# Kernel tuning notes

Measured on AMD Instinct MI355X. Metric: run time of the kernel, lower is better.

## Reference

```python
import jax, jax.numpy as jnp
import numpy as np
from functools import partial

# norse LIFAdEx default parameters
DT = 0.001
TAU_SYN_INV = 1.0 / 5e-3   # 200.0
TAU_MEM_INV = 1.0 / 1e-2   # 100.0
TAU_ADA_INV = 2.0
ADAPT_CURRENT = 4.0
ADAPT_SPIKE = 0.02
DELTA_T = 0.5
V_LEAK = 0.0
V_TH = 1.0
V_RESET = 0.0
ALPHA = 100.0              # superspike surrogate sharpness
TAU_FILTER_INV = 223.1435511314


@jax.custom_vjp
def superspike(x):
    # forward: heaviside; backward: superspike surrogate grad
    return (x > 0).astype(x.dtype)

def _ss_fwd(x):
    return superspike(x), x

def _ss_bwd(x, g):
    return (g / (ALPHA * jnp.abs(x) + 1.0) ** 2,)

superspike.defvjp(_ss_fwd, _ss_bwd)


def lif_adex_recurrent(x, W_in, W_rec):
    """x: (T,B,F) -> spikes (T,B,H). norse lif_adex_step semantics."""
    T, B, _ = x.shape
    H = W_rec.shape[0]
    # precompute feed-forward input current for all steps: (T,B,H)
    i_in = jnp.einsum('tbf,hf->tbh', x, W_in)

    def step(carry, ic):
        z, v, i, a = carry
        dv = DT * TAU_MEM_INV * ((V_LEAK - v)
                                 + DELTA_T * jnp.exp((v - V_TH) / DELTA_T)
                                 + i - a)
        v_dec = v + dv
        i_dec = i - DT * TAU_SYN_INV * i
        a_dec = a + DT * TAU_ADA_INV * (ADAPT_CURRENT * (v - V_LEAK) - a)
        z_new = superspike(v_dec - V_TH)
        v_new = (1.0 - z_new) * v_dec + z_new * V_RESET
        i_new = i_dec + ic + z @ W_rec.T
        a_new = a_dec + z_new * ADAPT_SPIKE
        return (z_new, v_new, i_new, a_new), z_new

    z0 = jnp.zeros((B, H), x.dtype)
    init = (z0, z0, z0, z0)
    _, spikes = jax.lax.scan(step, init, i_in)
    return spikes


def exp_filter(spikes, W_out, b_out):
    """Linear readout + exponential low-pass filter over time."""
    y = jnp.einsum('tbh,oh->tbo', spikes, W_out) + b_out  # (T,B,O)
    k = DT * TAU_FILTER_INV

    def step(o_prev, y_t):
        o = o_prev + k * (y_t - o_prev)
        return o, o

    o0 = y[0]
    _, rest = jax.lax.scan(step, o0, y[1:])
    return jnp.concatenate([o0[None], rest], axis=0)


def setup_inputs() -> dict:
    key = jax.random.key(0)
    kx, k1, k2, k3, k4 = jax.random.split(key, 5)
    T, B, F, H, O = 500, 128, 128, 512, 32
    x = jax.random.normal(kx, (T, B, F), dtype=jnp.float32)
    W_in = jax.random.normal(k1, (H, F), dtype=jnp.float32) * np.sqrt(2.0 / F)
    W_rec = jax.random.normal(k2, (H, H), dtype=jnp.float32) * np.sqrt(2.0 / H)
    W_out = jax.random.normal(k3, (O, H), dtype=jnp.float32) * np.sqrt(1.0 / H)
    b_out = jax.random.normal(k4, (O,), dtype=jnp.float32) * 0.01
    return {'x': x, 'W_in': W_in, 'W_rec': W_rec, 'W_out': W_out, 'b_out': b_out}


def reference(x, W_in, W_rec, W_out, b_out):
    spikes = lif_adex_recurrent(x, W_in, W_rec)
    return exp_filter(spikes, W_out, b_out)
```

## Files before the change

### kernel.cpp

```cpp
#include <hip/hip_runtime.h>
#include <hip/hip_bf16.h>
#include <cstdint>
#include <cstddef>

#define T_STEPS 500
#define BATCH   128
#define FDIM    128
#define HDIM    512
#define ODIM    32
#define M_ROWS  (T_STEPS * BATCH)
#define ZOFF    (512u << 11)

__device__ __forceinline__ float bfbits2f(unsigned short u) {
    union { unsigned int i; float f; } c; c.i = ((unsigned int)u) << 16; return c.f;
}

__global__ void detect_kernel(const unsigned short* __restrict__ xw, int* __restrict__ flag) {
    __shared__ int cnt;
    if (threadIdx.x == 0) cnt = 0;
    __syncthreads();
    unsigned short w = xw[threadIdx.x * 2];
    int e = (w >> 7) & 0xFF;
    if (e >= 170) atomicAdd(&cnt, 1);
    __syncthreads();
    if (threadIdx.x == 0) *flag = (cnt >= 8) ? 1 : 0;
}

__global__ void prep_kernel(const void* __restrict__ Wrec,
                            const void* __restrict__ Wout,
                            const void* __restrict__ bout,
                            const void* __restrict__ Win,
                            const int* __restrict__ flag,
                            float* __restrict__ WrecT,
                            float* __restrict__ WoutT,
                            float* __restrict__ WinT,
                            float* __restrict__ bout32) {
    const int fp32 = *flag;
    int idx = blockIdx.x * blockDim.x + threadIdx.x;
    if (idx < HDIM * HDIM) {
        int h  = idx / HDIM;
        int hp = idx % HDIM;
        float v = fp32 ? ((const float*)Wrec)[idx]
                       : bfbits2f(((const unsigned short*)Wrec)[idx]);
        WrecT[hp * HDIM + h] = v;
    }
    if (idx < HDIM) WrecT[HDIM * HDIM + idx] = 0.f;
    if (idx < ODIM * HDIM) {
        int o = idx / HDIM;
        int h = idx % HDIM;
        float v = fp32 ? ((const float*)Wout)[idx]
                       : bfbits2f(((const unsigned short*)Wout)[idx]);
        WoutT[h * ODIM + o] = v;
    }
    if (idx < HDIM * FDIM) {
        int h = idx / FDIM;
        int f = idx % FDIM;
        float v = fp32 ? ((const float*)Win)[idx]
                       : bfbits2f(((const unsigned short*)Win)[idx]);
        WinT[f * HDIM + h] = v;
    }
    if (idx < ODIM) {
        bout32[idx] = fp32 ? ((const float*)bout)[idx]
                           : bfbits2f(((const unsigned short*)bout)[idx]);
    }
}

__global__ __launch_bounds__(256) void iin_gemm(const void* __restrict__ x,
                                                const float* __restrict__ WinT,
                                                const int* __restrict__ flag,
                                                float* __restrict__ iin) {
    const int fp32 = *flag;
    const int tid  = threadIdx.x;
    const int m0   = blockIdx.x * 32;

    __shared__ float xs[32][FDIM];

    for (int i = tid; i < 32 * FDIM; i += 256) {
        size_t g = (size_t)m0 * FDIM + i;
        xs[0][i] = fp32 ? ((const float*)x)[g]
                        : bfbits2f(((const unsigned short*)x)[g]);
    }
    __syncthreads();

    float acc[32][2];
#pragma unroll
    for (int m = 0; m < 32; ++m) { acc[m][0] = 0.f; acc[m][1] = 0.f; }

#pragma unroll 4
    for (int k = 0; k < FDIM; ++k) {
        float w0 = WinT[(size_t)k * HDIM + tid];
        float w1 = WinT[(size_t)k * HDIM + 256 + tid];
#pragma unroll
        for (int m = 0; m < 32; ++m) {
            float xv = xs[m][k];
            acc[m][0] += xv * w0;
            acc[m][1] += xv * w1;
        }
    }

#pragma unroll
    for (int m = 0; m < 32; ++m) {
        iin[(size_t)(m0 + m) * HDIM + tid]       = acc[m][0];
        iin[(size_t)(m0 + m) * HDIM + 256 + tid] = acc[m][1];
    }
}

__global__ __launch_bounds__(1024) void scan_kernel(const float* __restrict__ iin,
                                                    const float* __restrict__ WrecT,
                                                    unsigned long long* __restrict__ masksG) {
    const int b    = blockIdx.x;
    const int tid  = threadIdx.x;
    const int q    = tid & 127;
    const int p    = tid >> 7;
    const int lane = tid & 63;
    const int wv   = tid >> 6;
    const bool st  = tid < HDIM;
    const int h    = tid;

    __shared__ unsigned long long wmask[8];
    __shared__ float4 part[8][128];
    __shared__ alignas(16) unsigned int slA[8][68];
    __shared__ alignas(16) unsigned int slB[8][68];
    unsigned int (*slO)[68] = slA;
    unsigned int (*slN)[68] = slB;

    const float kDvC  = 0.1f;
    const float kSyn  = 0.2f;
    const float kAda  = 0.002f;

    float v = 0.f, cur = 0.f, a = 0.f;
    int   cnt = 0;
    const char* WQ = (const char*)WrecT + q * 16;

    for (int t = 0; t < T_STEPS; ++t) {
        float ic = 0.f, i_dec = 0.f;
        bool  zk = false;
        unsigned long long m = 0;

        if (st) {
            ic = iin[((size_t)t * BATCH + b) * HDIM + h];
            float s = (0.0f - v) + 0.5f * expf((v - 1.0f) * 2.0f);
            s = s + cur;
            s = s - a;
            float v_dec = v + kDvC * s;
            i_dec = cur - kSyn * cur;
            float a_dec = a + kAda * (4.0f * v - a);
            zk = (v_dec - 1.0f) > 0.0f;

            m = __ballot(zk);
            if (lane == 0) {
                wmask[wv] = m;
                masksG[((size_t)t * BATCH + b) * 8 + wv] = m;
            }
            v = zk ? 0.0f : v_dec;
            a = zk ? (a_dec + 0.02f) : a_dec;
        }

        float4 rs = {0.f, 0.f, 0.f, 0.f};
        {
            const int n  = (cnt + 7 - p) >> 3;
            const int ng = (n + 3) >> 2;
            float4 b0[4], b1[4];
            auto ld4 = [&](int g, float4* d) {
                uint4 i0 = *(const uint4*)&slO[p][g << 2];
                d[0] = *(const float4*)(WQ + i0.x);
                d[1] = *(const float4*)(WQ + i0.y);
                d[2] = *(const float4*)(WQ + i0.z);
                d[3] = *(const float4*)(WQ + i0.w);
            };
            auto acc4 = [&](const float4* d) {
#pragma unroll
                for (int u = 0; u < 4; ++u) {
                    rs.x += d[u].x; rs.y += d[u].y; rs.z += d[u].z; rs.w += d[u].w;
                }
            };
            int g = 0;
            if (ng > 0) ld4(0, b0);
            while (g + 2 <= ng) {
                ld4(g + 1, b1);
                acc4(b0);
                if (g + 2 < ng) ld4(g + 2, b0);
                acc4(b1);
                g += 2;
            }
            if (g < ng) acc4(b0);
        }
        part[p][q] = rs;

        __syncthreads();

        int total = 0;
#pragma unroll
        for (int w = 0; w < 8; ++w) total += __popcll(wmask[w]);

        if (st) {
            float rec = 0.f;
#pragma unroll
            for (int pp = 0; pp < 8; ++pp)
                rec += ((const float*)&part[pp][h >> 2])[h & 3];
            cur = (i_dec + ic) + rec;

            if (zk) {
                int off = __popcll(m & ((1ull << lane) - 1ull));
#pragma unroll
                for (int w = 0; w < 8; ++w)
                    if (w < wv) off += __popcll(wmask[w]);
                slN[off & 7][off >> 3] = (unsigned int)h << 11;
            }
        } else if (tid < HDIM + 32) {
            int s  = (tid - HDIM) >> 2;
            int k  = (tid - HDIM) & 3;
            int ne = (total + 7 - s) >> 3;
            int padc = (4 - (ne & 3)) & 3;
            if (k < padc) slN[s][ne + k] = ZOFF;
        }
        cnt = total;

        __syncthreads();

        unsigned int (*tp)[68] = slO; slO = slN; slN = tp;
    }
}

__global__ __launch_bounds__(256) void y_kernel(const unsigned long long* __restrict__ masks,
                                                const float* __restrict__ WoutT,
                                                const float* __restrict__ bout,
                                                float* __restrict__ y) {
    const int tid = threadIdx.x;
    const int p   = blockIdx.x * 8 + (tid >> 5);
    const int o   = tid & 31;
    const unsigned long long* mp = masks + (size_t)p * 8;
    float acc = 0.f;
#pragma unroll
    for (int w = 0; w < 8; ++w) {
        unsigned long long m = mp[w];
        const float* Wb = WoutT + (size_t)w * 64 * ODIM + o;
        while (m) {
            int j = __builtin_ctzll(m);
            acc += Wb[j * ODIM];
            m &= m - 1;
        }
    }
    y[(size_t)p * ODIM + o] = acc + bout[o];
}

__global__ __launch_bounds__(64) void filter_kernel(const float* __restrict__ y,
                                                    const int* __restrict__ flag,
                                                    void* __restrict__ out) {
    const int p = blockIdx.x * 64 + threadIdx.x;
    const int fp32o = *flag;
    const float kf = 0.2231435511314f;
    float c0[10], c1[10];
#pragma unroll
    for (int u = 0; u < 10; ++u) c0[u] = y[(size_t)u * (BATCH * ODIM) + p];
    float o_state = 0.f;
    for (int base = 0; base < T_STEPS; base += 10) {
        if (base + 10 < T_STEPS) {
#pragma unroll
            for (int u = 0; u < 10; ++u)
                c1[u] = y[(size_t)(base + 10 + u) * (BATCH * ODIM) + p];
        }
#pragma unroll
        for (int u = 0; u < 10; ++u) {
            int t = base + u;
            float yt = c0[u];
            o_state = (t == 0) ? yt : (o_state + kf * (yt - o_state));
            size_t oi = (size_t)t * (BATCH * ODIM) + p;
            if (fp32o) ((float*)out)[oi] = o_state;
            else       ((__hip_bfloat16*)out)[oi] = __float2bfloat16(o_state);
        }
#pragma unroll
        for (int u = 0; u < 10; ++u) c0[u] = c1[u];
    }
}

extern "C" void kernel_launch(void* const* d_in, const int* in_sizes, int n_in,
                              void* d_out, int out_size, void* d_ws, size_t ws_size,
                              hipStream_t stream) {
    const void* x = d_in[0]; const void* Win = d_in[1]; const void* Wrec = d_in[2];
    const void* Wout = d_in[3]; const void* bout = d_in[4];
    for (int i = 0; i < n_in; ++i) {
        switch (in_sizes[i]) {
            case 8192000: x    = d_in[i]; break;
            case 65536:   Win  = d_in[i]; break;
            case 262144:  Wrec = d_in[i]; break;
            case 16384:   Wout = d_in[i]; break;
            case 32:      bout = d_in[i]; break;
            default: break;
        }
    }

    const size_t OFF_FLAG  = 0;
    const size_t OFF_BOUT  = 256;
    const size_t OFF_WOUTT = 512;
    const size_t OFF_WRECT = 66048;
    const size_t OFF_WINT  = 1116672;
    const size_t OFF_MASK  = 1378816;
    const size_t OFF_IIN   = 5474816;
    const size_t OFF_Y     = OFF_IIN;
    const size_t REQUIRED  = OFF_IIN + (size_t)M_ROWS * HDIM * 4;
    if (ws_size < REQUIRED) return;

    char* ws = (char*)d_ws;
    int*    flag   = (int*)(ws + OFF_FLAG);
    float*  bout32 = (float*)(ws + OFF_BOUT);
    float*  WoutT  = (float*)(ws + OFF_WOUTT);
    float*  WrecT  = (float*)(ws + OFF_WRECT);
    float*  WinT   = (float*)(ws + OFF_WINT);
    unsigned long long* masks = (unsigned long long*)(ws + OFF_MASK);
    float*  iin    = (float*)(ws + OFF_IIN);
    float*  y      = (float*)(ws + OFF_Y);

    hipLaunchKernelGGL(detect_kernel, dim3(1), dim3(256), 0, stream,
                       (const unsigned short*)x, flag);
    hipLaunchKernelGGL(prep_kernel, dim3((HDIM * HDIM + 255) / 256), dim3(256), 0, stream,
                       Wrec, Wout, bout, Win, flag, WrecT, WoutT, WinT, bout32);
    hipLaunchKernelGGL(iin_gemm, dim3(M_ROWS / 32), dim3(256), 0, stream,
                       x, WinT, flag, iin);
    hipLaunchKernelGGL(scan_kernel, dim3(BATCH), dim3(1024), 0, stream,
                       iin, WrecT, masks);
    hipLaunchKernelGGL(y_kernel, dim3(M_ROWS / 8), dim3(256), 0, stream,
                       masks, WoutT, bout32, y);
    hipLaunchKernelGGL(filter_kernel, dim3((BATCH * ODIM) / 64), dim3(64), 0, stream,
                       y, flag, d_out);
}
```

Before: 906.8 us.

## Add bf16 paths: MFMA input GEMM and bf16 recurrent weights in scan

When inputs are bf16 (detected at runtime), the input-current GEMM runs on MFMA bf16 instructions instead of a scalar fp32 VALU loop. The recurrent scan gathers bf16-packed transposed W_rec rows, halving the bytes per spike gather, with a 16-way split of the spike list and a software prefetch of the next step's input current. Barriers now wait only on LDS counters instead of a full __syncthreads. Both paths are launched and each exits early depending on the flag, which adds an extra empty kernel launch per stage.

```diff
diff --git a/kernel.cpp b/kernel.cpp
--- a/kernel.cpp
+++ b/kernel.cpp
@@ -10,9 +10,20 @@
 #define ODIM    32
 #define M_ROWS  (T_STEPS * BATCH)
 #define ZOFF    (512u << 11)
+#define ZOFFB   (512u << 10)
+
+typedef __attribute__((ext_vector_type(8))) __bf16 bf16x8;
+typedef __attribute__((ext_vector_type(4))) float  f32x4;
 
 __device__ __forceinline__ float bfbits2f(unsigned short u) {
     union { unsigned int i; float f; } c; c.i = ((unsigned int)u) << 16; return c.f;
+}
+__device__ __forceinline__ float asf(unsigned int u) {
+    union { unsigned int i; float f; } c; c.i = u; return c.f;
+}
+__device__ __forceinline__ void lds_barrier() {
+    asm volatile("s_waitcnt lgkmcnt(0)" ::: "memory");
+    __builtin_amdgcn_s_barrier();
 }
 
 __global__ void detect_kernel(const unsigned short* __restrict__ xw, int* __restrict__ flag) {
@@ -32,54 +43,88 @@
                             const void* __restrict__ Win,
                             const int* __restrict__ flag,
                             float* __restrict__ WrecT,
+                            unsigned short* __restrict__ WrecTb,
                             float* __restrict__ WoutT,
                             float* __restrict__ WinT,
                             float* __restrict__ bout32) {
     const int fp32 = *flag;
     int idx = blockIdx.x * blockDim.x + threadIdx.x;
-    if (idx < HDIM * HDIM) {
-        int h  = idx / HDIM;
-        int hp = idx % HDIM;
-        float v = fp32 ? ((const float*)Wrec)[idx]
-                       : bfbits2f(((const unsigned short*)Wrec)[idx]);
-        WrecT[hp * HDIM + h] = v;
-    }
-    if (idx < HDIM) WrecT[HDIM * HDIM + idx] = 0.f;
+    if (fp32) {
+        if (idx < HDIM * HDIM) {
+            int h = idx / HDIM, hp = idx % HDIM;
+            WrecT[hp * HDIM + h] = ((const float*)Wrec)[idx];
+        }
+        if (idx < HDIM) WrecT[HDIM * HDIM + idx] = 0.f;
+        if (idx < HDIM * FDIM) {
+            int h = idx / FDIM, f = idx % FDIM;
+            WinT[f * HDIM + h] = ((const float*)Win)[idx];
+        }
+    } else {
+        if (idx < HDIM * HDIM) {
+            int h = idx / HDIM, hp = idx % HDIM;
+            WrecTb[hp * HDIM + h] = ((const unsigned short*)Wrec)[idx];
+        }
+        if (idx < HDIM) WrecTb[HDIM * HDIM + idx] = 0;
+    }
     if (idx < ODIM * HDIM) {
-        int o = idx / HDIM;
-        int h = idx % HDIM;
-        float v = fp32 ? ((const float*)Wout)[idx]
-                       : bfbits2f(((const unsigned short*)Wout)[idx]);
-        WoutT[h * ODIM + o] = v;
-    }
-    if (idx < HDIM * FDIM) {
-        int h = idx / FDIM;
-        int f = idx % FDIM;
-        float v = fp32 ? ((const float*)Win)[idx]
-                       : bfbits2f(((const unsigned short*)Win)[idx]);
-        WinT[f * HDIM + h] = v;
-    }
-    if (idx < ODIM) {
+        int o = idx / HDIM, h = idx % HDIM;
+        WoutT[h * ODIM + o] = fp32 ? ((const float*)Wout)[idx]
+                                   : bfbits2f(((const unsigned short*)Wout)[idx]);
+    }
+    if (idx < ODIM)
         bout32[idx] = fp32 ? ((const float*)bout)[idx]
                            : bfbits2f(((const unsigned short*)bout)[idx]);
-    }
-}
-
-__global__ __launch_bounds__(256) void iin_gemm(const void* __restrict__ x,
-                                                const float* __restrict__ WinT,
-                                                const int* __restrict__ flag,
-                                                float* __restrict__ iin) {
-    const int fp32 = *flag;
+}
+
+__global__ __launch_bounds__(256) void iin_gemm_mfma(const __hip_bfloat16* __restrict__ x,
+                                                     const __hip_bfloat16* __restrict__ Win,
+                                                     const int* __restrict__ flag,
+                                                     float* __restrict__ iin) {
+    if (*flag != 0) return;
+    const int mt   = blockIdx.x;
+    const int nt   = blockIdx.y;
+    const int wave = threadIdx.x >> 6;
+    const int lane = threadIdx.x & 63;
+    const int l15  = lane & 15;
+    const int quad = lane >> 4;
+    const int m_base = mt * 64 + wave * 16;
+    const int n_base = nt * 64;
+
+    const __bf16* xb = reinterpret_cast<const __bf16*>(x);
+    const __bf16* wb = reinterpret_cast<const __bf16*>(Win);
+
+    f32x4 acc[4] = {{0.f,0.f,0.f,0.f},{0.f,0.f,0.f,0.f},{0.f,0.f,0.f,0.f},{0.f,0.f,0.f,0.f}};
+
+#pragma unroll
+    for (int kk = 0; kk < 4; ++kk) {
+        const int k0 = kk * 32 + quad * 8;
+        bf16x8 a = *reinterpret_cast<const bf16x8*>(xb + (size_t)(m_base + l15) * FDIM + k0);
+#pragma unroll
+        for (int nb = 0; nb < 4; ++nb) {
+            bf16x8 bf = *reinterpret_cast<const bf16x8*>(wb + (size_t)(n_base + nb * 16 + l15) * FDIM + k0);
+            acc[nb] = __builtin_amdgcn_mfma_f32_16x16x32_bf16(a, bf, acc[nb], 0, 0, 0);
+        }
+    }
+
+#pragma unroll
+    for (int nb = 0; nb < 4; ++nb)
+#pragma unroll
+        for (int r = 0; r < 4; ++r)
+            iin[(size_t)(m_base + quad * 4 + r) * HDIM + n_base + nb * 16 + l15] = acc[nb][r];
+}
+
+__global__ __launch_bounds__(256) void iin_gemm_valu(const void* __restrict__ x,
+                                                     const float* __restrict__ WinT,
+                                                     const int* __restrict__ flag,
+                                                     float* __restrict__ iin) {
+    if (*flag != 1) return;
     const int tid  = threadIdx.x;
     const int m0   = blockIdx.x * 32;
 
     __shared__ float xs[32][FDIM];
 
-    for (int i = tid; i < 32 * FDIM; i += 256) {
-        size_t g = (size_t)m0 * FDIM + i;
-        xs[0][i] = fp32 ? ((const float*)x)[g]
-                        : bfbits2f(((const unsigned short*)x)[g]);
-    }
+    for (int i = tid; i < 32 * FDIM; i += 256)
+        xs[0][i] = ((const float*)x)[(size_t)m0 * FDIM + i];
     __syncthreads();
 
     float acc[32][2];
@@ -105,9 +150,137 @@
     }
 }
 
-__global__ __launch_bounds__(1024) void scan_kernel(const float* __restrict__ iin,
-                                                    const float* __restrict__ WrecT,
-                                                    unsigned long long* __restrict__ masksG) {
+__global__ __launch_bounds__(1024) void scan_bf16(const float* __restrict__ iin,
+                                                  const unsigned short* __restrict__ WrecTb,
+                                                  const int* __restrict__ flag,
+                                                  unsigned long long* __restrict__ masksG) {
+    if (*flag != 0) return;
+    const int b    = blockIdx.x;
+    const int tid  = threadIdx.x;
+    const int q    = tid & 63;
+    const int pc   = tid >> 6;
+    const int lane = tid & 63;
+    const int wv   = tid >> 6;
+    const bool st  = tid < HDIM;
+    const int h    = tid;
+
+    __shared__ unsigned long long wmask[8];
+    __shared__ float4 partA[16][64];
+    __shared__ float4 partB[16][64];
+    __shared__ alignas(16) unsigned int slA[16][36];
+    __shared__ alignas(16) unsigned int slB[16][36];
+    unsigned int (*slO)[36] = slA;
+    unsigned int (*slN)[36] = slB;
+
+    float v = 0.f, cur = 0.f, a = 0.f;
+    int   cnt = 0;
+    const char* WQ = (const char*)WrecTb + q * 16;
+    float ic_cur = st ? iin[(size_t)b * HDIM + h] : 0.f;
+
+    for (int t = 0; t < T_STEPS; ++t) {
+        float ic_next = 0.f;
+        if (st && (t + 1) < T_STEPS)
+            ic_next = iin[((size_t)(t + 1) * BATCH + b) * HDIM + h];
+
+        float i_dec = 0.f; bool zk = false; unsigned long long m = 0;
+        if (st) {
+            float s = (0.0f - v) + 0.5f * expf((v - 1.0f) * 2.0f);
+            s = s + cur;
+            s = s - a;
+            float v_dec = v + 0.1f * s;
+            i_dec = cur - 0.2f * cur;
+            float a_dec = a + 0.002f * (4.0f * v - a);
+            zk = (v_dec - 1.0f) > 0.0f;
+            m = __ballot(zk);
+            if (lane == 0) {
+                wmask[wv] = m;
+                masksG[((size_t)t * BATCH + b) * 8 + wv] = m;
+            }
+            v = zk ? 0.0f : v_dec;
+            a = zk ? (a_dec + 0.02f) : a_dec;
+        }
+
+        float rs0=0.f,rs1=0.f,rs2=0.f,rs3=0.f,rs4=0.f,rs5=0.f,rs6=0.f,rs7=0.f;
+        {
+            const unsigned int* sl = slO[pc];
+            const int n  = (cnt + 15 - pc) >> 4;
+            const int ng = (n + 3) >> 2;
+            uint4 w0[4], w1[4];
+            auto ldg = [&](int g, uint4* w) {
+                uint4 ix = *(const uint4*)(sl + (g << 2));
+                w[0] = *(const uint4*)(WQ + ix.x);
+                w[1] = *(const uint4*)(WQ + ix.y);
+                w[2] = *(const uint4*)(WQ + ix.z);
+                w[3] = *(const uint4*)(WQ + ix.w);
+            };
+            auto accw = [&](const uint4* w) {
+#pragma unroll
+                for (int u = 0; u < 4; ++u) {
+                    rs0 += asf(w[u].x << 16); rs1 += asf(w[u].x & 0xffff0000u);
+                    rs2 += asf(w[u].y << 16); rs3 += asf(w[u].y & 0xffff0000u);
+                    rs4 += asf(w[u].z << 16); rs5 += asf(w[u].z & 0xffff0000u);
+                    rs6 += asf(w[u].w << 16); rs7 += asf(w[u].w & 0xffff0000u);
+                }
+            };
+            int g = 0;
+            if (ng > 0) ldg(0, w0);
+            while (g + 2 <= ng) {
+                ldg(g + 1, w1);
+                accw(w0);
+                if (g + 2 < ng) ldg(g + 2, w0);
+                accw(w1);
+                g += 2;
+            }
+            if (g < ng) accw(w0);
+        }
+        partA[pc][q] = (float4){rs0, rs1, rs2, rs3};
+        partB[pc][q] = (float4){rs4, rs5, rs6, rs7};
+
+        lds_barrier();
+
+        int total = 0;
+#pragma unroll
+        for (int w = 0; w < 8; ++w) total += __popcll(wmask[w]);
+
+        if (st) {
+            float rec = 0.f;
+            const int  qq = h >> 3, jj = h & 3;
+            const bool hi = (h & 4) != 0;
+#pragma unroll
+            for (int pp = 0; pp < 16; ++pp) {
+                const float* pa = (const float*)&partA[pp][qq];
+                const float* pb = (const float*)&partB[pp][qq];
+                rec += hi ? pb[jj] : pa[jj];
+            }
+            cur = (i_dec + ic_cur) + rec;
+
+            if (zk) {
+                int off = __popcll(m & ((1ull << lane) - 1ull));
+#pragma unroll
+                for (int w = 0; w < 8; ++w) if (w < wv) off += __popcll(wmask[w]);
+                slN[off & 15][off >> 4] = (unsigned int)h << 10;
+            }
+        } else if (tid < HDIM + 64) {
+            int s5 = (tid - HDIM) >> 2;
+            int k  = (tid - HDIM) & 3;
+            int ne = (total + 15 - s5) >> 4;
+            int padc = (4 - (ne & 3)) & 3;
+            if (k < padc) slN[s5][ne + k] = ZOFFB;
+        }
+        cnt = total;
+        ic_cur = ic_next;
+
+        lds_barrier();
+
+        unsigned int (*tp)[36] = slO; slO = slN; slN = tp;
+    }
+}
+
+__global__ __launch_bounds__(1024) void scan_f32(const float* __restrict__ iin,
+                                                 const float* __restrict__ WrecT,
+                                                 const int* __restrict__ flag,
+                                                 unsigned long long* __restrict__ masksG) {
+    if (*flag != 1) return;
     const int b    = blockIdx.x;
     const int tid  = threadIdx.x;
     const int q    = tid & 127;
@@ -124,10 +297,6 @@
     unsigned int (*slO)[68] = slA;
     unsigned int (*slN)[68] = slB;
 
-    const float kDvC  = 0.1f;
-    const float kSyn  = 0.2f;
-    const float kAda  = 0.002f;
-
     float v = 0.f, cur = 0.f, a = 0.f;
     int   cnt = 0;
     const char* WQ = (const char*)WrecT + q * 16;
@@ -142,11 +311,10 @@
             float s = (0.0f - v) + 0.5f * expf((v - 1.0f) * 2.0f);
             s = s + cur;
             s = s - a;
-            float v_dec = v + kDvC * s;
-            i_dec = cur - kSyn * cur;
-            float a_dec = a + kAda * (4.0f * v - a);
+            float v_dec = v + 0.1f * s;
+            i_dec = cur - 0.2f * cur;
+            float a_dec = a + 0.002f * (4.0f * v - a);
             zk = (v_dec - 1.0f) > 0.0f;
-
             m = __ballot(zk);
             if (lane == 0) {
                 wmask[wv] = m;
@@ -199,20 +367,18 @@
             for (int pp = 0; pp < 8; ++pp)
                 rec += ((const float*)&part[pp][h >> 2])[h & 3];
             cur = (i_dec + ic) + rec;
-
             if (zk) {
                 int off = __popcll(m & ((1ull << lane) - 1ull));
 #pragma unroll
-                for (int w = 0; w < 8; ++w)
-                    if (w < wv) off += __popcll(wmask[w]);
+                for (int w = 0; w < 8; ++w) if (w < wv) off += __popcll(wmask[w]);
                 slN[off & 7][off >> 3] = (unsigned int)h << 11;
             }
         } else if (tid < HDIM + 32) {
-            int s  = (tid - HDIM) >> 2;
+            int s5 = (tid - HDIM) >> 2;
             int k  = (tid - HDIM) & 3;
-            int ne = (total + 7 - s) >> 3;
+            int ne = (total + 7 - s5) >> 3;
             int padc = (4 - (ne & 3)) & 3;
-            if (k < padc) slN[s][ne + k] = ZOFF;
+            if (k < padc) slN[s5][ne + k] = ZOFF;
         }
         cnt = total;
 
@@ -302,23 +468,28 @@
     if (ws_size < REQUIRED) return;
 
     char* ws = (char*)d_ws;
-    int*    flag   = (int*)(ws + OFF_FLAG);
-    float*  bout32 = (float*)(ws + OFF_BOUT);
-    float*  WoutT  = (float*)(ws + OFF_WOUTT);
-    float*  WrecT  = (float*)(ws + OFF_WRECT);
-    float*  WinT   = (float*)(ws + OFF_WINT);
+    int*            flag   = (int*)(ws + OFF_FLAG);
+    float*          bout32 = (float*)(ws + OFF_BOUT);
+    float*          WoutT  = (float*)(ws + OFF_WOUTT);
+    float*          WrecT  = (float*)(ws + OFF_WRECT);
+    unsigned short* WrecTb = (unsigned short*)(ws + OFF_WRECT);
+    float*          WinT   = (float*)(ws + OFF_WINT);
     unsigned long long* masks = (unsigned long long*)(ws + OFF_MASK);
-    float*  iin    = (float*)(ws + OFF_IIN);
-    float*  y      = (float*)(ws + OFF_Y);
+    float*          iin    = (float*)(ws + OFF_IIN);
+    float*          y      = (float*)(ws + OFF_Y);
 
     hipLaunchKernelGGL(detect_kernel, dim3(1), dim3(256), 0, stream,
                        (const unsigned short*)x, flag);
     hipLaunchKernelGGL(prep_kernel, dim3((HDIM * HDIM + 255) / 256), dim3(256), 0, stream,
-                       Wrec, Wout, bout, Win, flag, WrecT, WoutT, WinT, bout32);
-    hipLaunchKernelGGL(iin_gemm, dim3(M_ROWS / 32), dim3(256), 0, stream,
+                       Wrec, Wout, bout, Win, flag, WrecT, WrecTb, WoutT, WinT, bout32);
+    hipLaunchKernelGGL(iin_gemm_mfma, dim3(M_ROWS / 64, HDIM / 64), dim3(256), 0, stream,
+                       (const __hip_bfloat16*)x, (const __hip_bfloat16*)Win, flag, iin);
+    hipLaunchKernelGGL(iin_gemm_valu, dim3(M_ROWS / 32), dim3(256), 0, stream,
                        x, WinT, flag, iin);
-    hipLaunchKernelGGL(scan_kernel, dim3(BATCH), dim3(1024), 0, stream,
-                       iin, WrecT, masks);
+    hipLaunchKernelGGL(scan_bf16, dim3(BATCH), dim3(1024), 0, stream,
+                       iin, WrecTb, flag, masks);
+    hipLaunchKernelGGL(scan_f32, dim3(BATCH), dim3(1024), 0, stream,
+                       iin, WrecT, flag, masks);
     hipLaunchKernelGGL(y_kernel, dim3(M_ROWS / 8), dim3(256), 0, stream,
                        masks, WoutT, bout32, y);
     hipLaunchKernelGGL(filter_kernel, dim3((BATCH * ODIM) / 64), dim3(64), 0, stream,
```

Measured after the change: 904.2 us. About the same (-0.3%).
